# Performance work log

Hardware: AMD Instinct MI355X
Metric: run time of the kernel (lower is better)

Reference implementation:

```python
import jax, jax.numpy as jnp
import numpy as np

KS = 7                 # sconv_kernel_size
PAD = (KS - 1) // 2
SIMS_SCALE = 10.0      # sims_norm_scale
EPS = 1e-5


def setup_inputs() -> dict:
    key = jax.random.key(0)
    k1, k2, k3, k4 = jax.random.split(key, 4)
    T, C, H, W = 4, 3, 192, 192
    S = 300
    x = jax.random.normal(k1, (T, C, H, W), jnp.float32)
    spix = jax.random.randint(k2, (T, H, W), 0, S, dtype=jnp.int32)
    W_lin = jax.random.normal(k3, (C, C * KS * KS), jnp.float32) * 0.05
    b_lin = jax.random.normal(k4, (C,), jnp.float32) * 0.05
    return {"x": x, "spix": spix, "W_lin": W_lin, "b_lin": b_lin, "n_spix": S}


def _get_sims(x, spix, n_spix, scale):
    # x: [T,C,H,W], spix: [T,H,W] with contiguous ids in [0, n_spix)
    T, C, H, W = x.shape
    feats = x.transpose(0, 2, 3, 1).reshape(T, H * W, C)   # t (h w) f
    ids = spix.reshape(T, H * W)

    def pool(f, i):
        s = jax.ops.segment_sum(f, i, num_segments=n_spix)                      # [S,C]
        c = jax.ops.segment_sum(jnp.ones((f.shape[0],), f.dtype), i, num_segments=n_spix)  # [S]
        return s / jnp.maximum(c, 1.0)[:, None], c

    means, cnt = jax.vmap(pool)(feats, ids)                # [T,S,C], [T,S]
    # squared euclidean distance (cdist ** 2)
    d2 = (jnp.sum(feats * feats, -1)[:, :, None]
          + jnp.sum(means * means, -1)[:, None, :]
          - 2.0 * jnp.einsum('tnc,tsc->tns', feats, means))
    d2 = jnp.maximum(d2, 0.0)                              # [T,HW,S]
    # superpixels absent from frame t get distance inf (pwd[mask] = inf)
    d2 = jnp.where((cnt > 0)[:, None, :], d2, jnp.inf)
    sims = jax.nn.softmax(-scale * d2, axis=-1)            # softmax over superpixels
    return sims.reshape(T, H, W, n_spix)                   # [T,H,W,S]


def _prod_attn(sims):
    # non-local 'prod' search, zero flow, ws=KS: dot product of sims vectors
    # between each pixel and its KSxKS neighborhood (zero-padded borders)
    T, H, W, S = sims.shape
    p = jnp.pad(sims, ((0, 0), (PAD, PAD), (PAD, PAD), (0, 0)))
    attn = [jnp.einsum('thws,thws->thw', sims, p[:, dy:dy + H, dx:dx + W, :])
            for dy in range(KS) for dx in range(KS)]
    return jnp.stack(attn, -1)                             # [T,H,W,KS*KS]


def _unfold(x):
    # torch.nn.Unfold(kernel_size=KS, padding=PAD): zero pad, row-major window
    T, C, H, W = x.shape
    p = jnp.pad(x, ((0, 0), (0, 0), (PAD, PAD), (PAD, PAD)))
    pats = [p[:, :, dy:dy + H, dx:dx + W] for dy in range(KS) for dx in range(KS)]
    return jnp.stack(pats, 2)                              # [T,C,KS*KS,H,W]


def reference(x, spix, W_lin, b_lin, n_spix):
    T, C, H, W = x.shape
    sims = _get_sims(x, spix, n_spix, SIMS_SCALE)          # [T,H,W,S]
    rw = _prod_attn(sims)                                  # [T,H,W,K2]
    # apply_norm('max'): divide by max over neighborhood
    rw = rw / (EPS + jnp.max(rw, axis=-1, keepdims=True))
    Wk = W_lin.reshape(W_lin.shape[0], C, KS * KS)         # [od,id,k2]
    pats = _unfold(x)                                      # [T,id,k2,H,W]
    # out[t,o,h,w] = sum_{i,k} W[o,i,k] * rw[t,h,w,k] * patch[t,i,k,h,w] + b[o]
    out = jnp.einsum('oik,thwk,tikhw->tohw', Wk, rw, pats) + b_lin[None, :, None, None]
    return out
```

## Files before the change

kernel.cpp:

```cpp
#include <hip/hip_runtime.h>
#include <math.h>

#define TT 4
#define HH 192
#define WW 192
#define SS 300
#define SP 320
#define HW (HH*WW)
#define PD 3
#define HSZ 22
#define NHP 484
#define NG 1936
#define LOG2E 1.44269504088896340736f
#define MEANS 81920
#define MOFF 98304
#define ZOFF (MOFF + TT*HW)

typedef _Float16 h8 __attribute__((ext_vector_type(8)));
typedef float f4 __attribute__((ext_vector_type(4)));


__launch_bounds__(256)
__global__ void k_accum(const float* __restrict__ x, const int* __restrict__ spix,
                        float* __restrict__ ws) {
    __shared__ float ls[SS * 4];
    const int tid = threadIdx.x;
    const int t = blockIdx.y, seg = blockIdx.x;
    for (int i = tid; i < SS * 4; i += 256) ls[i] = 0.f;
    __syncthreads();
    const int pb = seg * 2304 + tid * 9;
    const int* sp = spix + t * HW + pb;
    const float* x0 = x + (t * 3 + 0) * HW + pb;
    const float* x1 = x + (t * 3 + 1) * HW + pb;
    const float* x2 = x + (t * 3 + 2) * HW + pb;
    float a0 = 0.f, a1 = 0.f, a2 = 0.f, ac = 0.f;
    int scur = sp[0];
#pragma unroll
    for (int it = 0; it < 9; it++) {
        int s = sp[it];
        if (s != scur) {
            atomicAdd(&ls[scur * 4 + 0], a0);
            atomicAdd(&ls[scur * 4 + 1], a1);
            atomicAdd(&ls[scur * 4 + 2], a2);
            atomicAdd(&ls[scur * 4 + 3], ac);
            scur = s; a0 = a1 = a2 = ac = 0.f;
        }
        a0 += x0[it]; a1 += x1[it]; a2 += x2[it]; ac += 1.f;
    }
    atomicAdd(&ls[scur * 4 + 0], a0);
    atomicAdd(&ls[scur * 4 + 1], a1);
    atomicAdd(&ls[scur * 4 + 2], a2);
    atomicAdd(&ls[scur * 4 + 3], ac);
    __syncthreads();
    float* part = ws + (t * 16 + seg) * 1200;
    for (int i = tid; i < SS * 4; i += 256) part[i] = ls[i];
}

__launch_bounds__(256)
__global__ void k_prep(const float* __restrict__ x, float* __restrict__ ws) {
    __shared__ float4 sm[SP];
    const int tid = threadIdx.x;
    const int t = blockIdx.y;
    const float* part = ws + t * 16 * 1200;
    for (int i = tid; i < SP; i += 256) {
        float4 m;
        if (i < SS) {
            float s0 = 0.f, s1 = 0.f, s2 = 0.f, c = 0.f;
#pragma unroll
            for (int g = 0; g < 16; g++) {
                s0 += part[g * 1200 + i * 4 + 0];
                s1 += part[g * 1200 + i * 4 + 1];
                s2 += part[g * 1200 + i * 4 + 2];
                c  += part[g * 1200 + i * 4 + 3];
            }
            float inv = 1.f / fmaxf(c, 1.f);
            float mx = s0 * inv, my = s1 * inv, mz = s2 * inv;
            m.x = 20.f * LOG2E * mx; m.y = 20.f * LOG2E * my; m.z = 20.f * LOG2E * mz;
            m.w = (c > 0.f) ? (-10.f * LOG2E * (mx * mx + my * my + mz * mz)) : -INFINITY;
        } else {
            m.x = 0.f; m.y = 0.f; m.z = 0.f; m.w = -INFINITY;
        }
        sm[i] = m;
        if (blockIdx.x == 0) ((float4*)(ws + MEANS))[t * SP + i] = m;
    }
    __syncthreads();

    const int p0 = blockIdx.x * 512 + tid;
    const int p1 = p0 + 256;
    const float f0x = x[(t * 3 + 0) * HW + p0], f0y = x[(t * 3 + 1) * HW + p0], f0z = x[(t * 3 + 2) * HW + p0];
    const float f1x = x[(t * 3 + 0) * HW + p1], f1y = x[(t * 3 + 1) * HW + p1], f1z = x[(t * 3 + 2) * HW + p1];

    float M0 = -INFINITY, M1 = -INFINITY;
#pragma unroll 4
    for (int s = 0; s < SS; s++) {
        float4 a = sm[s];
        M0 = fmaxf(M0, fmaf(f0x, a.x, fmaf(f0y, a.y, fmaf(f0z, a.z, a.w))));
        M1 = fmaxf(M1, fmaf(f1x, a.x, fmaf(f1y, a.y, fmaf(f1z, a.z, a.w))));
    }
    float Z0 = 0.f, Z1 = 0.f;
#pragma unroll 4
    for (int s = 0; s < SS; s++) {
        float4 a = sm[s];
        Z0 += exp2f(fmaf(f0x, a.x, fmaf(f0y, a.y, fmaf(f0z, a.z, a.w))) - M0);
        Z1 += exp2f(fmaf(f1x, a.x, fmaf(f1y, a.y, fmaf(f1z, a.z, a.w))) - M1);
    }
    ws[MOFF + t * HW + p0] = M0;
    ws[MOFF + t * HW + p1] = M1;
    ws[ZOFF + t * HW + p0] = 1.f / Z0;
    ws[ZOFF + t * HW + p1] = 1.f / Z1;
}

#define REP49(M) M(0)M(1)M(2)M(3)M(4)M(5)M(6)M(7)M(8)M(9)M(10)M(11)M(12)M(13) \
    M(14)M(15)M(16)M(17)M(18)M(19)M(20)M(21)M(22)M(23)M(24)M(25)M(26)M(27) \
    M(28)M(29)M(30)M(31)M(32)M(33)M(34)M(35)M(36)M(37)M(38)M(39)M(40)M(41) \
    M(42)M(43)M(44)M(45)M(46)M(47)M(48)

#define QOFF(k) (((k) / 7 - PD) * HSZ + ((k) % 7 - PD))


__launch_bounds__(512, 2)
__global__ void k_main(const float* __restrict__ x, const float* __restrict__ Wlin,
                       const float* __restrict__ blin, const float* __restrict__ ws,
                       float* __restrict__ out) {
    __shared__ __align__(16) char ebuf[2][NG * 16];
    __shared__ float4 sfh[NHP];
    __shared__ float  sW[441];
    __shared__ float4 smean[SP];

    const int tid = threadIdx.x;
    const int wid = tid >> 6, lane = tid & 63;
    const int pxc = lane & 15, kg = lane >> 4;
    const int t = blockIdx.z;
    const int gx0 = blockIdx.x * 16 - PD, gy0 = blockIdx.y * 16 - PD;
    const float4* m4 = (const float4*)(ws + MEANS) + t * SP;

    for (int i = tid; i < 441; i += 512) sW[i] = Wlin[i];
    for (int i = tid; i < SP; i += 512) smean[i] = m4[i];

    float fx = 0.f, fy = 0.f, fz = 0.f, M = INFINITY;
    if (tid < NHP) {
        int hy = tid / HSZ, hx = tid - hy * HSZ;
        int gy = gy0 + hy, gx = gx0 + hx;
        float iZ = 0.f;
        if (gy >= 0 && gy < HH && gx >= 0 && gx < WW) {
            int p = gy * WW + gx;
            fx = x[(t * 3 + 0) * HW + p];
            fy = x[(t * 3 + 1) * HW + p];
            fz = x[(t * 3 + 2) * HW + p];
            M  = ws[MOFF + t * HW + p];
            iZ = ws[ZOFF + t * HW + p];
        }
        sfh[tid] = make_float4(fx, fy, fz, iZ);
    }
    __syncthreads();

#define PHASEB(cc, bb) if (tid < NHP) { \
        char* dst = ebuf[bb]; \
        _Pragma("unroll") \
        for (int jd = 0; jd < 4; jd++) { \
            h8 v; \
            _Pragma("unroll") \
            for (int e = 0; e < 4; e++) { \
                float4 ma = smean[(cc) * 32 + jd * 8 + 2 * e]; \
                float4 mb = smean[(cc) * 32 + jd * 8 + 2 * e + 1]; \
                float E0 = exp2f(fmaf(fx, ma.x, fmaf(fy, ma.y, fmaf(fz, ma.z, ma.w))) - M); \
                float E1 = exp2f(fmaf(fx, mb.x, fmaf(fy, mb.y, fmaf(fz, mb.z, mb.w))) - M); \
                auto pr = __builtin_amdgcn_cvt_pkrtz(E0, E1); \
                v[2 * e] = (_Float16)pr.x; v[2 * e + 1] = (_Float16)pr.y; \
            } \
            *(h8*)(dst + (jd * NHP + tid) * 16) = v; \
        } }

    const int r0 = 2 * wid;
    const int gA0 = kg * NHP + (r0 + PD) * HSZ + PD + pxc;
    const int gA1 = gA0 + HSZ;
    const int bcol2 = (16 + pxc > 21) ? 21 : 16 + pxc;
    const int gB1 = kg * NHP + r0 * HSZ + pxc;
    const int gB2 = kg * NHP + r0 * HSZ + bcol2;

    f4 zero4 = {0.f, 0.f, 0.f, 0.f};
    f4 aP[7], aQ[7], aR[7], aS[7];
#pragma unroll
    for (int d = 0; d < 7; d++) { aP[d] = zero4; aQ[d] = zero4; aR[d] = zero4; aS[d] = zero4; }

    PHASEB(0, 0)

#pragma unroll 1
    for (int c = 0; c < 10; c++) {
        __syncthreads();
        if (c < 9) { PHASEB(c + 1, (c + 1) & 1) }
        const char* pb = ebuf[c & 1];
        h8 A0 = *(const h8*)(pb + gA0 * 16);
        h8 A1 = *(const h8*)(pb + gA1 * 16);
        h8 b1 = *(const h8*)(pb + gB1 * 16);
        h8 b2 = *(const h8*)(pb + gB2 * 16);
        aP[0] = __builtin_amdgcn_mfma_f32_16x16x32_f16(A0, b1, aP[0], 0, 0, 0);
        aQ[0] = __builtin_amdgcn_mfma_f32_16x16x32_f16(A0, b2, aQ[0], 0, 0, 0);
#pragma unroll
        for (int d = 1; d < 7; d++) {
            h8 n1 = *(const h8*)(pb + (gB1 + d * HSZ) * 16);
            h8 n2 = *(const h8*)(pb + (gB2 + d * HSZ) * 16);
            aP[d]     = __builtin_amdgcn_mfma_f32_16x16x32_f16(A0, n1, aP[d], 0, 0, 0);
            aR[d - 1] = __builtin_amdgcn_mfma_f32_16x16x32_f16(A1, n1, aR[d - 1], 0, 0, 0);
            aQ[d]     = __builtin_amdgcn_mfma_f32_16x16x32_f16(A0, n2, aQ[d], 0, 0, 0);
            aS[d - 1] = __builtin_amdgcn_mfma_f32_16x16x32_f16(A1, n2, aS[d - 1], 0, 0, 0);
        }
        h8 l1 = *(const h8*)(pb + (gB1 + 7 * HSZ) * 16);
        h8 l2 = *(const h8*)(pb + (gB2 + 7 * HSZ) * 16);
        aR[6] = __builtin_amdgcn_mfma_f32_16x16x32_f16(A1, l1, aR[6], 0, 0, 0);
        aS[6] = __builtin_amdgcn_mfma_f32_16x16x32_f16(A1, l2, aS[6], 0, 0, 0);
    }
    __syncthreads();

    float* attn = (float*)ebuf;
#pragma unroll
    for (int d = 0; d < 7; d++) {
#pragma unroll
        for (int reg = 0; reg < 4; reg++) {
            int i = 4 * kg + reg;
            int u1 = pxc - i;
            int u2 = u1 + 16;
            if ((unsigned)u1 <= 6u) {
                attn[(r0 * 16 + i) * 51 + d * 7 + u1] = aP[d][reg];
                attn[((r0 + 1) * 16 + i) * 51 + d * 7 + u1] = aR[d][reg];
            }
            if ((unsigned)u2 <= 6u) {
                attn[(r0 * 16 + i) * 51 + d * 7 + u2] = aQ[d][reg];
                attn[((r0 + 1) * 16 + i) * 51 + d * 7 + u2] = aS[d][reg];
            }
        }
    }
    __syncthreads();

    if (tid < 256) {
        const int r = tid >> 4, cq = tid & 15;
        const int own = (r + PD) * HSZ + (cq + PD);
        const float* ap = attn + tid * 51;
        float mx = 0.f;
#define PK1(k) mx = fmaxf(mx, ap[k] * sfh[own + QOFF(k)].w);
        REP49(PK1)
#undef PK1
        const float iZp = sfh[own].w;
        const float inv = 1.f / (1e-5f / iZp + mx);

        float o0 = blin[0], o1 = blin[1], o2 = blin[2];
#define PK2(k) { float4 f = sfh[own + QOFF(k)]; \
        float rwk = ap[k] * f.w * inv; \
        o0 += rwk * (sW[k] * f.x + sW[49 + (k)] * f.y + sW[98 + (k)] * f.z); \
        o1 += rwk * (sW[147 + (k)] * f.x + sW[196 + (k)] * f.y + sW[245 + (k)] * f.z); \
        o2 += rwk * (sW[294 + (k)] * f.x + sW[343 + (k)] * f.y + sW[392 + (k)] * f.z); }
        REP49(PK2)
#undef PK2

        int p = (gy0 + PD + r) * WW + gx0 + PD + cq;
        out[(t * 3 + 0) * HW + p] = o0;
        out[(t * 3 + 1) * HW + p] = o1;
        out[(t * 3 + 2) * HW + p] = o2;
    }
}

extern "C" void kernel_launch(void* const* d_in, const int* in_sizes, int n_in,
                              void* d_out, int out_size, void* d_ws, size_t ws_size,
                              hipStream_t stream) {
    (void)in_sizes; (void)n_in; (void)out_size; (void)ws_size;
    const float* x    = (const float*)d_in[0];
    const int*   spix = (const int*)d_in[1];
    const float* Wlin = (const float*)d_in[2];
    const float* blin = (const float*)d_in[3];
    float* out = (float*)d_out;
    float* ws  = (float*)d_ws;

    hipLaunchKernelGGL(k_accum, dim3(16, TT), dim3(256), 0, stream, x, spix, ws);
    hipLaunchKernelGGL(k_prep,  dim3(HW / 512, TT), dim3(256), 0, stream, x, ws);
    hipLaunchKernelGGL(k_main,  dim3(WW / 16, HH / 16, TT), dim3(512), 0, stream,
                       x, Wlin, blin, ws, out);
}
```

Measured before the change: 135.9 us.

## Split accumulation over more blocks, pad LDS stride, stagger MFMA/exp phases across waves

The accumulation kernel now uses 72 segments per frame with two pixels per thread and direct shared atomics, replacing 16 segments with run-length merging. This raises parallelism but makes the prep reduction loop over 72 partials instead of 16. In the main kernel the per-group LDS stride is padded from 484 to 486 entries to reduce bank conflicts. Odd and even waves swap the order of the MFMA chunk and the exp-generation phase, with s_setprio around the MFMAs, so matrix and VALU work from different waves can overlap.

New measurement: 133.0 us. 2.1% less time.

```diff
diff --git a/kernel.cpp b/kernel.cpp
--- a/kernel.cpp
+++ b/kernel.cpp
@@ -10,10 +10,11 @@
 #define PD 3
 #define HSZ 22
 #define NHP 484
-#define NG 1936
+#define PSTRG 486
 #define LOG2E 1.44269504088896340736f
-#define MEANS 81920
-#define MOFF 98304
+#define NSEG 72
+#define MEANS 360448
+#define MOFF 393216
 #define ZOFF (MOFF + TT*HW)
 
 typedef _Float16 h8 __attribute__((ext_vector_type(8)));
@@ -28,31 +29,17 @@
     const int t = blockIdx.y, seg = blockIdx.x;
     for (int i = tid; i < SS * 4; i += 256) ls[i] = 0.f;
     __syncthreads();
-    const int pb = seg * 2304 + tid * 9;
-    const int* sp = spix + t * HW + pb;
-    const float* x0 = x + (t * 3 + 0) * HW + pb;
-    const float* x1 = x + (t * 3 + 1) * HW + pb;
-    const float* x2 = x + (t * 3 + 2) * HW + pb;
-    float a0 = 0.f, a1 = 0.f, a2 = 0.f, ac = 0.f;
-    int scur = sp[0];
-#pragma unroll
-    for (int it = 0; it < 9; it++) {
-        int s = sp[it];
-        if (s != scur) {
-            atomicAdd(&ls[scur * 4 + 0], a0);
-            atomicAdd(&ls[scur * 4 + 1], a1);
-            atomicAdd(&ls[scur * 4 + 2], a2);
-            atomicAdd(&ls[scur * 4 + 3], ac);
-            scur = s; a0 = a1 = a2 = ac = 0.f;
-        }
-        a0 += x0[it]; a1 += x1[it]; a2 += x2[it]; ac += 1.f;
-    }
-    atomicAdd(&ls[scur * 4 + 0], a0);
-    atomicAdd(&ls[scur * 4 + 1], a1);
-    atomicAdd(&ls[scur * 4 + 2], a2);
-    atomicAdd(&ls[scur * 4 + 3], ac);
-    __syncthreads();
-    float* part = ws + (t * 16 + seg) * 1200;
+    const int pb = seg * 512 + tid * 2;
+#pragma unroll
+    for (int it = 0; it < 2; it++) {
+        int s = spix[t * HW + pb + it];
+        atomicAdd(&ls[s * 4 + 0], x[(t * 3 + 0) * HW + pb + it]);
+        atomicAdd(&ls[s * 4 + 1], x[(t * 3 + 1) * HW + pb + it]);
+        atomicAdd(&ls[s * 4 + 2], x[(t * 3 + 2) * HW + pb + it]);
+        atomicAdd(&ls[s * 4 + 3], 1.f);
+    }
+    __syncthreads();
+    float* part = ws + (t * NSEG + seg) * 1200;
     for (int i = tid; i < SS * 4; i += 256) part[i] = ls[i];
 }
 
@@ -61,13 +48,12 @@
     __shared__ float4 sm[SP];
     const int tid = threadIdx.x;
     const int t = blockIdx.y;
-    const float* part = ws + t * 16 * 1200;
+    const float* part = ws + t * NSEG * 1200;
     for (int i = tid; i < SP; i += 256) {
         float4 m;
         if (i < SS) {
             float s0 = 0.f, s1 = 0.f, s2 = 0.f, c = 0.f;
-#pragma unroll
-            for (int g = 0; g < 16; g++) {
+            for (int g = 0; g < NSEG; g++) {
                 s0 += part[g * 1200 + i * 4 + 0];
                 s1 += part[g * 1200 + i * 4 + 1];
                 s2 += part[g * 1200 + i * 4 + 2];
@@ -122,7 +108,7 @@
 __global__ void k_main(const float* __restrict__ x, const float* __restrict__ Wlin,
                        const float* __restrict__ blin, const float* __restrict__ ws,
                        float* __restrict__ out) {
-    __shared__ __align__(16) char ebuf[2][NG * 16];
+    __shared__ __align__(16) char ebuf[2][4 * PSTRG * 16];
     __shared__ float4 sfh[NHP];
     __shared__ float  sW[441];
     __shared__ float4 smean[SP];
@@ -168,47 +154,57 @@
                 auto pr = __builtin_amdgcn_cvt_pkrtz(E0, E1); \
                 v[2 * e] = (_Float16)pr.x; v[2 * e + 1] = (_Float16)pr.y; \
             } \
-            *(h8*)(dst + (jd * NHP + tid) * 16) = v; \
+            *(h8*)(dst + (jd * PSTRG + tid) * 16) = v; \
         } }
 
     const int r0 = 2 * wid;
-    const int gA0 = kg * NHP + (r0 + PD) * HSZ + PD + pxc;
+    const int gA0 = kg * PSTRG + (r0 + PD) * HSZ + PD + pxc;
     const int gA1 = gA0 + HSZ;
     const int bcol2 = (16 + pxc > 21) ? 21 : 16 + pxc;
-    const int gB1 = kg * NHP + r0 * HSZ + pxc;
-    const int gB2 = kg * NHP + r0 * HSZ + bcol2;
+    const int gB1 = kg * PSTRG + r0 * HSZ + pxc;
+    const int gB2 = kg * PSTRG + r0 * HSZ + bcol2;
 
     f4 zero4 = {0.f, 0.f, 0.f, 0.f};
     f4 aP[7], aQ[7], aR[7], aS[7];
 #pragma unroll
     for (int d = 0; d < 7; d++) { aP[d] = zero4; aQ[d] = zero4; aR[d] = zero4; aS[d] = zero4; }
+
+#define MFMA_CHUNK { \
+        __builtin_amdgcn_s_setprio(1); \
+        h8 A0 = *(const h8*)(pb + gA0 * 16); \
+        h8 A1 = *(const h8*)(pb + gA1 * 16); \
+        h8 b1 = *(const h8*)(pb + gB1 * 16); \
+        h8 b2 = *(const h8*)(pb + gB2 * 16); \
+        aP[0] = __builtin_amdgcn_mfma_f32_16x16x32_f16(A0, b1, aP[0], 0, 0, 0); \
+        aQ[0] = __builtin_amdgcn_mfma_f32_16x16x32_f16(A0, b2, aQ[0], 0, 0, 0); \
+        _Pragma("unroll") \
+        for (int d = 1; d < 7; d++) { \
+            h8 n1 = *(const h8*)(pb + (gB1 + d * HSZ) * 16); \
+            h8 n2 = *(const h8*)(pb + (gB2 + d * HSZ) * 16); \
+            aP[d]     = __builtin_amdgcn_mfma_f32_16x16x32_f16(A0, n1, aP[d], 0, 0, 0); \
+            aR[d - 1] = __builtin_amdgcn_mfma_f32_16x16x32_f16(A1, n1, aR[d - 1], 0, 0, 0); \
+            aQ[d]     = __builtin_amdgcn_mfma_f32_16x16x32_f16(A0, n2, aQ[d], 0, 0, 0); \
+            aS[d - 1] = __builtin_amdgcn_mfma_f32_16x16x32_f16(A1, n2, aS[d - 1], 0, 0, 0); \
+        } \
+        h8 l1 = *(const h8*)(pb + (gB1 + 7 * HSZ) * 16); \
+        h8 l2 = *(const h8*)(pb + (gB2 + 7 * HSZ) * 16); \
+        aR[6] = __builtin_amdgcn_mfma_f32_16x16x32_f16(A1, l1, aR[6], 0, 0, 0); \
+        aS[6] = __builtin_amdgcn_mfma_f32_16x16x32_f16(A1, l2, aS[6], 0, 0, 0); \
+        __builtin_amdgcn_s_setprio(0); }
 
     PHASEB(0, 0)
 
 #pragma unroll 1
     for (int c = 0; c < 10; c++) {
         __syncthreads();
-        if (c < 9) { PHASEB(c + 1, (c + 1) & 1) }
         const char* pb = ebuf[c & 1];
-        h8 A0 = *(const h8*)(pb + gA0 * 16);
-        h8 A1 = *(const h8*)(pb + gA1 * 16);
-        h8 b1 = *(const h8*)(pb + gB1 * 16);
-        h8 b2 = *(const h8*)(pb + gB2 * 16);
-        aP[0] = __builtin_amdgcn_mfma_f32_16x16x32_f16(A0, b1, aP[0], 0, 0, 0);
-        aQ[0] = __builtin_amdgcn_mfma_f32_16x16x32_f16(A0, b2, aQ[0], 0, 0, 0);
-#pragma unroll
-        for (int d = 1; d < 7; d++) {
-            h8 n1 = *(const h8*)(pb + (gB1 + d * HSZ) * 16);
-            h8 n2 = *(const h8*)(pb + (gB2 + d * HSZ) * 16);
-            aP[d]     = __builtin_amdgcn_mfma_f32_16x16x32_f16(A0, n1, aP[d], 0, 0, 0);
-            aR[d - 1] = __builtin_amdgcn_mfma_f32_16x16x32_f16(A1, n1, aR[d - 1], 0, 0, 0);
-            aQ[d]     = __builtin_amdgcn_mfma_f32_16x16x32_f16(A0, n2, aQ[d], 0, 0, 0);
-            aS[d - 1] = __builtin_amdgcn_mfma_f32_16x16x32_f16(A1, n2, aS[d - 1], 0, 0, 0);
-        }
-        h8 l1 = *(const h8*)(pb + (gB1 + 7 * HSZ) * 16);
-        h8 l2 = *(const h8*)(pb + (gB2 + 7 * HSZ) * 16);
-        aR[6] = __builtin_amdgcn_mfma_f32_16x16x32_f16(A1, l1, aR[6], 0, 0, 0);
-        aS[6] = __builtin_amdgcn_mfma_f32_16x16x32_f16(A1, l2, aS[6], 0, 0, 0);
+        if (wid & 1) {
+            MFMA_CHUNK
+            if (c < 9) { PHASEB(c + 1, (c + 1) & 1) }
+        } else {
+            if (c < 9) { PHASEB(c + 1, (c + 1) & 1) }
+            MFMA_CHUNK
+        }
     }
     __syncthreads();
 
@@ -270,7 +266,7 @@
     float* out = (float*)d_out;
     float* ws  = (float*)d_ws;
 
-    hipLaunchKernelGGL(k_accum, dim3(16, TT), dim3(256), 0, stream, x, spix, ws);
+    hipLaunchKernelGGL(k_accum, dim3(NSEG, TT), dim3(256), 0, stream, x, spix, ws);
     hipLaunchKernelGGL(k_prep,  dim3(HW / 512, TT), dim3(256), 0, stream, x, ws);
     hipLaunchKernelGGL(k_main,  dim3(WW / 16, HH / 16, TT), dim3(512), 0, stream,
                        x, Wlin, blin, ws, out);
```
